# Kernel tuning notes

Measured on AMD Instinct MI355X. Metric: run time of the kernel, lower is better.

## Reference

```python
import jax, jax.numpy as jnp
import numpy as np

B, S, D = 4, 1024, 1024
H, DK, DV = 16, 64, 64


def setup_inputs() -> dict:
    key = jax.random.key(0)
    ks = jax.random.split(key, 8)
    sc = 0.02
    return {
        "queries": jax.random.normal(ks[0], (B, S, D), jnp.float32),
        "keys": jax.random.normal(ks[1], (B, S, D), jnp.float32),
        "values": jax.random.normal(ks[2], (B, S, D), jnp.float32),
        "attn_bias": jax.random.normal(ks[3], (B, 1, S, S), jnp.float32),
        "Wq": jax.random.normal(ks[4], (H * DK, D), jnp.float32) * sc,
        "Wk": jax.random.normal(ks[5], (H * DK, D), jnp.float32) * sc,
        "Wv": jax.random.normal(ks[6], (H * DV, D), jnp.float32) * sc,
        "Wp": jax.random.normal(ks[7], (D, H * DV), jnp.float32) * sc,
    }


def reference(queries, keys, values, attn_bias, Wq, Wk, Wv, Wp):
    # Linear (no bias): x @ W.T, then split heads -> [B, H, S, d]
    q = (queries @ Wq.T).reshape(B, S, H, DK).transpose(0, 2, 1, 3)
    k = (keys @ Wk.T).reshape(B, S, H, DK).transpose(0, 2, 1, 3)
    v = (values @ Wv.T).reshape(B, S, H, DV).transpose(0, 2, 1, 3)
    # NOTE: original scales by d_model**-0.5, not d_key**-0.5
    scores = jnp.einsum("bhqd,bhkd->bhqk", q, k) * (D ** -0.5)
    scores = scores + attn_bias  # bias broadcasts over heads
    weights = jax.nn.softmax(scores, axis=-1)
    out = jnp.einsum("bhqk,bhkd->bhqd", weights, v)  # [B,H,S,DV]
    out = out.transpose(0, 2, 1, 3).reshape(B, S, H * DV)
    return out @ Wp.T
```

## Files before the change

kernel.cpp:

```cpp
#include <hip/hip_runtime.h>
#include <hip/hip_bf16.h>

typedef unsigned short u16;
typedef unsigned int u32;
typedef __attribute__((ext_vector_type(8))) short bf16x8;
typedef __attribute__((ext_vector_type(8))) u16 u16x8;
typedef __attribute__((ext_vector_type(4))) u16 u16x4;
typedef __attribute__((ext_vector_type(4))) u32 u32x4;
typedef __attribute__((ext_vector_type(4))) float f32x4;
typedef __attribute__((ext_vector_type(16))) float f32x16;

typedef const __attribute__((address_space(1))) void* gas1_t;
typedef __attribute__((address_space(3))) void* las3_t;

#define MFMA16(a,b,c) __builtin_amdgcn_mfma_f32_16x16x32_bf16((a),(b),(c),0,0,0)
#define MFMA32(a,b,c) __builtin_amdgcn_mfma_f32_32x32x16_bf16((a),(b),(c),0,0,0)

static constexpr int BB = 4, SS = 1024, DD = 1024, HH = 16;

static __device__ __forceinline__ u16 f2b(float x) {
  union { __hip_bfloat16 h; u16 u; } cv;
  cv.h = __float2bfloat16(x);
  return cv.u;
}
static __device__ __forceinline__ u32 pk2(float a, float b) {
  return (u32)f2b(a) | ((u32)f2b(b) << 16);
}

__global__ __launch_bounds__(256) void cvt_all(
    const float* __restrict__ q, const float* __restrict__ k, const float* __restrict__ v,
    const float* __restrict__ wq_, const float* __restrict__ wk_, const float* __restrict__ wv_,
    const float* __restrict__ wp_,
    u16* __restrict__ qb, u16* __restrict__ kb, u16* __restrict__ vb,
    u16* __restrict__ wqb, u16* __restrict__ wkb, u16* __restrict__ wvb, u16* __restrict__ wpb) {
  int bid = blockIdx.x;
  const float* s; u16* d; int off;
  if      (bid < 4096)  { s = q;   d = qb;  off = bid; }
  else if (bid < 8192)  { s = k;   d = kb;  off = bid - 4096; }
  else if (bid < 12288) { s = v;   d = vb;  off = bid - 8192; }
  else if (bid < 13312) { s = wq_; d = wqb; off = bid - 12288; }
  else if (bid < 14336) { s = wk_; d = wkb; off = bid - 13312; }
  else if (bid < 15360) { s = wv_; d = wvb; off = bid - 14336; }
  else                  { s = wp_; d = wpb; off = bid - 15360; }
  int i = (off * 256 + threadIdx.x) * 4;
  float4 val = *(const float4*)(s + i);
  u16x4 r = { f2b(val.x), f2b(val.y), f2b(val.z), f2b(val.w) };
  *(u16x4*)(d + i) = r;
}

template<typename OT>
__global__ __launch_bounds__(256) void gemm_bt(
    const u16* __restrict__ Abase, const u16* __restrict__ Wbase, OT* __restrict__ Cbase,
    int N, int K, size_t sA, size_t sW, size_t sC) {
  const u16* A = Abase + (size_t)blockIdx.z * sA;
  const u16* W = Wbase + (size_t)blockIdx.z * sW;
  OT* C = Cbase + (size_t)blockIdx.z * sC;

  __shared__ __align__(16) u16 As[128 * 32];
  __shared__ __align__(16) u16 Bs[128 * 32];

  const int tid = threadIdx.x;
  const int lane = tid & 63;
  const int wid = tid >> 6;
  const int g = lane >> 4;
  const int li = lane & 15;
  const int brow = blockIdx.y * 128;
  const int bcol = blockIdx.x * 128;
  const int wr = (wid >> 1) * 64;
  const int wc = (wid & 1) * 64;

  const int srow = tid >> 2;
  const int scol = (tid & 3) * 8;

  f32x4 acc[4][4] = {};

  for (int k0 = 0; k0 < K; k0 += 32) {
#pragma unroll
    for (int c = 0; c < 2; ++c) {
      const u16* ga = A + (size_t)(brow + srow + c * 64) * K + k0 + scol;
      const u16* gw = W + (size_t)(bcol + srow + c * 64) * K + k0 + scol;
      __builtin_amdgcn_global_load_lds((gas1_t)(const void*)ga,
                                       (las3_t)(void*)(As + wid * 512 + c * 2048), 16, 0, 0);
      __builtin_amdgcn_global_load_lds((gas1_t)(const void*)gw,
                                       (las3_t)(void*)(Bs + wid * 512 + c * 2048), 16, 0, 0);
    }
    __syncthreads();

    bf16x8 a[4], b[4];
#pragma unroll
    for (int m = 0; m < 4; ++m)
      a[m] = *(const bf16x8*)&As[(wr + m * 16 + li) * 32 + g * 8];
#pragma unroll
    for (int n = 0; n < 4; ++n)
      b[n] = *(const bf16x8*)&Bs[(wc + n * 16 + li) * 32 + g * 8];
#pragma unroll
    for (int m = 0; m < 4; ++m)
#pragma unroll
      for (int n = 0; n < 4; ++n)
        acc[m][n] = MFMA16(a[m], b[n], acc[m][n]);
    __syncthreads();
  }

#pragma unroll
  for (int m = 0; m < 4; ++m)
#pragma unroll
    for (int n = 0; n < 4; ++n)
#pragma unroll
      for (int j = 0; j < 4; ++j) {
        int r = brow + wr + m * 16 + g * 4 + j;
        int c = bcol + wc + n * 16 + li;
        if constexpr (sizeof(OT) == 2) C[(size_t)r * N + c] = (OT)f2b(acc[m][n][j]);
        else                           C[(size_t)r * N + c] = acc[m][n][j];
      }
}

__global__ __launch_bounds__(256) void transpose_v(const u16* __restrict__ V, u16* __restrict__ Vt) {
  __shared__ __align__(16) u16 t[64][72];
  const int s0 = blockIdx.x * 64, h = blockIdx.y, b = blockIdx.z;
  const int tid = threadIdx.x;
#pragma unroll
  for (int it = 0; it < 2; ++it) {
    int slot = tid + it * 256;
    int r = slot >> 3, seg = slot & 7;
    *(u16x8*)&t[r][seg * 8] = *(const u16x8*)&V[(size_t)(b * SS + s0 + r) * DD + h * 64 + seg * 8];
  }
  __syncthreads();
#pragma unroll
  for (int it = 0; it < 2; ++it) {
    int slot = tid + it * 256;
    int dv = slot >> 3, seg = slot & 7;
    u16x8 v;
#pragma unroll
    for (int i = 0; i < 8; ++i) v[i] = t[seg * 8 + i][dv];
    *(u16x8*)&Vt[(size_t)((b * HH + h) * 64 + dv) * SS + s0 + seg * 8] = v;
  }
}

__global__ __launch_bounds__(256) void attn_kernel(
    const u16* __restrict__ Q, const u16* __restrict__ K, const u16* __restrict__ Vt,
    const float* __restrict__ bias, u16* __restrict__ O) {
  __shared__ __align__(16) u16 kbuf[2][64 * 64];
  __shared__ __align__(16) u16 vbuf[2][64 * 64];
  __shared__ float Lf[4][32];

  const int tid = threadIdx.x;
  const int lane = tid & 63;
  const int wq = tid >> 6;
  const int hi = lane >> 5;
  const int ln = lane & 31;
  const u32 swz = (u32)(ln & 7) << 4;
  const int h = blockIdx.y, b = blockIdx.z;
  const int q0 = blockIdx.x * 128;
  const int qrow = q0 + wq * 32 + ln;

  bf16x8 qf[4];
  {
    const u16* qp = Q + (size_t)(b * SS + qrow) * DD + h * 64 + hi * 8;
#pragma unroll
    for (int d = 0; d < 4; ++d) qf[d] = *(const bf16x8*)(qp + d * 16);
  }

  const int sr = tid >> 2;
  const int scb = (tid & 3) * 32;
  const u16* kg = K + (size_t)(b * SS + sr) * DD + h * 64 + scb / 2;
  const u16* vg = Vt + (size_t)((b * HH + h) * 64 + sr) * SS + scb / 2;
  const u32 wa0 = (u32)sr * 128 + (((u32)scb) ^ ((u32)(sr & 7) << 4));
  const u32 wa1 = (u32)sr * 128 + (((u32)scb + 16) ^ ((u32)(sr & 7) << 4));

  u16x8 kr0, kr1, vr0, vr1;
  kr0 = *(const u16x8*)(kg + 0);
  kr1 = *(const u16x8*)(kg + 8);
  vr0 = *(const u16x8*)(vg + 0);
  vr1 = *(const u16x8*)(vg + 8);
  *(u16x8*)((char*)kbuf[0] + wa0) = kr0;
  *(u16x8*)((char*)kbuf[0] + wa1) = kr1;
  *(u16x8*)((char*)vbuf[0] + wa0) = vr0;
  *(u16x8*)((char*)vbuf[0] + wa1) = vr1;
  __syncthreads();

  f32x16 o0 = {}, o1 = {};
  float m = -1e30f, lsum = 0.f;
  int cur = 0;

  for (int kt = 0; kt < 16; ++kt) {
    if (kt < 15) {
      const size_t k1 = (size_t)(kt + 1) * 64;
      kr0 = *(const u16x8*)(kg + k1 * DD + 0);
      kr1 = *(const u16x8*)(kg + k1 * DD + 8);
      vr0 = *(const u16x8*)(vg + k1 + 0);
      vr1 = *(const u16x8*)(vg + k1 + 8);
    }

    f32x4 bb[2][4];
    {
      const float* bp = bias + (size_t)(b * SS + qrow) * SS + kt * 64 + hi * 4;
#pragma unroll
      for (int kb = 0; kb < 2; ++kb)
#pragma unroll
        for (int rq = 0; rq < 4; ++rq)
          bb[kb][rq] = *(const f32x4*)(bp + kb * 32 + rq * 8);
    }

    const char* kb_base = (const char*)kbuf[cur];
    f32x16 s[2];
#pragma unroll
    for (int kb = 0; kb < 2; ++kb) {
      f32x16 acc = {};
#pragma unroll
      for (int d = 0; d < 4; ++d) {
        bf16x8 kf = *(const bf16x8*)(kb_base + (kb * 32 + ln) * 128 + (((u32)(d * 32 + hi * 16)) ^ swz));
        acc = MFMA32(kf, qf[d], acc);
      }
      s[kb] = acc;
    }
#pragma unroll
    for (int kb = 0; kb < 2; ++kb)
#pragma unroll
      for (int rq = 0; rq < 4; ++rq)
#pragma unroll
        for (int c = 0; c < 4; ++c)
          s[kb][rq * 4 + c] = fmaf(s[kb][rq * 4 + c], 0.03125f, bb[kb][rq][c]);

    float mt = -1e30f;
#pragma unroll
    for (int r = 0; r < 16; ++r) { mt = fmaxf(mt, s[0][r]); mt = fmaxf(mt, s[1][r]); }
    mt = fmaxf(mt, __shfl_xor(mt, 32));

    bool resc = false;
    float fsc = 1.f;
    if (kt == 0) {
      m = mt;
    } else if (__any(mt > m + 8.f)) {
      float mn = fmaxf(m, mt);
      fsc = __expf(m - mn);
      m = mn;
      resc = true;
    }

    float rs = 0.f;
    u32 w[2][8];
#pragma unroll
    for (int kb = 0; kb < 2; ++kb)
#pragma unroll
      for (int t = 0; t < 8; ++t) {
        float p0 = __expf(s[kb][2 * t] - m);
        float p1 = __expf(s[kb][2 * t + 1] - m);
        rs += p0 + p1;
        w[kb][t] = pk2(p0, p1);
      }
    rs += __shfl_xor(rs, 32);
    lsum = lsum * fsc + rs;

    if (resc) {
      if (hi == 0) Lf[wq][ln] = fsc;
#pragma unroll
      for (int rq = 0; rq < 4; ++rq) {
        f32x4 fv = *(const f32x4*)&Lf[wq][rq * 8 + hi * 4];
#pragma unroll
        for (int c = 0; c < 4; ++c) { o0[rq * 4 + c] *= fv[c]; o1[rq * 4 + c] *= fv[c]; }
      }
    }

    const char* vb_base = (const char*)vbuf[cur];
#pragma unroll
    for (int ks = 0; ks < 4; ++ks) {
      const int kb = ks >> 1, i0 = (ks & 1) * 4;
      u32 sA = hi ? w[kb][i0 + 0] : w[kb][i0 + 2];
      u32 sB = hi ? w[kb][i0 + 1] : w[kb][i0 + 3];
      u32 rA = (u32)__shfl_xor((int)sA, 32);
      u32 rB = (u32)__shfl_xor((int)sB, 32);
      u32 e0 = hi ? rA : w[kb][i0 + 0];
      u32 e1 = hi ? rB : w[kb][i0 + 1];
      u32 e2 = hi ? w[kb][i0 + 2] : rA;
      u32 e3 = hi ? w[kb][i0 + 3] : rB;
      union { u32x4 u; bf16x8 v; } pc;
      pc.u = (u32x4){e0, e1, e2, e3};
      bf16x8 pa = pc.v;
#pragma unroll
      for (int nv = 0; nv < 2; ++nv) {
        bf16x8 vf = *(const bf16x8*)(vb_base + (nv * 32 + ln) * 128 + (((u32)(ks * 32 + hi * 16)) ^ swz));
        if (nv == 0) o0 = MFMA32(pa, vf, o0);
        else         o1 = MFMA32(pa, vf, o1);
      }
    }

    if (kt < 15) {
      char* kd = (char*)kbuf[cur ^ 1];
      char* vd = (char*)vbuf[cur ^ 1];
      *(u16x8*)(kd + wa0) = kr0;
      *(u16x8*)(kd + wa1) = kr1;
      *(u16x8*)(vd + wa0) = vr0;
      *(u16x8*)(vd + wa1) = vr1;
      __syncthreads();
      cur ^= 1;
    }
  }

  float inv = 1.0f / lsum;
  if (hi == 0) Lf[wq][ln] = inv;
#pragma unroll
  for (int rq = 0; rq < 4; ++rq) {
    f32x4 iv = *(const f32x4*)&Lf[wq][rq * 8 + hi * 4];
#pragma unroll
    for (int c = 0; c < 4; ++c) {
      int q = q0 + wq * 32 + rq * 8 + hi * 4 + c;
      u16* op = O + (size_t)(b * SS + q) * DD + h * 64 + ln;
      op[0]  = f2b(o0[rq * 4 + c] * iv[c]);
      op[32] = f2b(o1[rq * 4 + c] * iv[c]);
    }
  }
}

extern "C" void kernel_launch(void* const* d_in, const int* in_sizes, int n_in,
                              void* d_out, int out_size, void* d_ws, size_t ws_size,
                              hipStream_t stream) {
  const float* queries = (const float*)d_in[0];
  const float* keys    = (const float*)d_in[1];
  const float* values  = (const float*)d_in[2];
  const float* bias    = (const float*)d_in[3];
  const float* Wq      = (const float*)d_in[4];
  const float* Wk      = (const float*)d_in[5];
  const float* Wv      = (const float*)d_in[6];
  const float* Wp      = (const float*)d_in[7];
  float* out = (float*)d_out;

  char* ws = (char*)d_ws;
  const size_t MB = 1024 * 1024;
  u16* qb  = (u16*)(ws + 0 * MB);
  u16* kb  = (u16*)(ws + 8 * MB);
  u16* vb  = (u16*)(ws + 16 * MB);
  u16* wqb = (u16*)(ws + 24 * MB);
  u16* wkb = (u16*)(ws + 26 * MB);
  u16* wvb = (u16*)(ws + 28 * MB);
  u16* wpb = (u16*)(ws + 30 * MB);
  u16* Qb  = (u16*)(ws + 32 * MB);
  u16* Kb  = (u16*)(ws + 40 * MB);
  u16* Vb  = (u16*)(ws + 48 * MB);
  u16* Vtb = (u16*)(ws + 56 * MB);
  u16* Ob  = (u16*)(ws + 0 * MB);

  const int nAct = BB * SS * DD;
  const int nW = DD * DD;

  cvt_all<<<dim3(16384), dim3(256), 0, stream>>>(
      queries, keys, values, Wq, Wk, Wv, Wp,
      qb, kb, vb, wqb, wkb, wvb, wpb);

  gemm_bt<u16><<<dim3(8, 32, 3), dim3(256), 0, stream>>>(
      qb, wqb, Qb, DD, DD, (size_t)nAct, (size_t)nW, (size_t)nAct);

  transpose_v<<<dim3(16, 16, 4), dim3(256), 0, stream>>>(Vb, Vtb);

  attn_kernel<<<dim3(8, 16, 4), dim3(256), 0, stream>>>(Qb, Kb, Vtb, bias, Ob);

  gemm_bt<float><<<dim3(8, 32, 1), dim3(256), 0, stream>>>(
      Ob, wpb, out, DD, DD, 0, 0, 0);
}
```

Measured before the change: 139.8 us.

## Prefetch attention bias one tile ahead and streamline softmax arithmetic

The attention bias tile for the next key block is now loaded into registers one iteration early, alongside the K/V prefetch, instead of right before use, so its global-memory latency is hidden. The softmax now uses exp2 with a folded log2e multiply-add, tree reductions for the row max and row sum, and a packed bf16 convert instruction in place of two scalar conversions. MFMA sections are wrapped in s_setprio raises to favour matrix issue across waves. The cost is an extra 32 live VGPRs for the prefetched bias, which may lower occupancy.

```diff
diff --git a/kernel.cpp b/kernel.cpp
--- a/kernel.cpp
+++ b/kernel.cpp
@@ -1,5 +1,6 @@
 #include <hip/hip_runtime.h>
 #include <hip/hip_bf16.h>
+#include <cmath>
 
 typedef unsigned short u16;
 typedef unsigned int u32;
@@ -23,8 +24,13 @@
   cv.h = __float2bfloat16(x);
   return cv.u;
 }
-static __device__ __forceinline__ u32 pk2(float a, float b) {
-  return (u32)f2b(a) | ((u32)f2b(b) << 16);
+static __device__ __forceinline__ u32 cvtpk(float lo, float hi) {
+  u32 r;
+  asm("v_cvt_pk_bf16_f32 %0, %1, %2" : "=v"(r) : "v"(lo), "v"(hi));
+  return r;
+}
+static __device__ __forceinline__ float fmax3(float a, float b, float c) {
+  return fmaxf(fmaxf(a, b), c);
 }
 
 __global__ __launch_bounds__(256) void cvt_all(
@@ -176,11 +182,21 @@
   *(u16x8*)((char*)kbuf[0] + wa1) = kr1;
   *(u16x8*)((char*)vbuf[0] + wa0) = vr0;
   *(u16x8*)((char*)vbuf[0] + wa1) = vr1;
+
+  const float* bp = bias + (size_t)(b * SS + qrow) * SS + hi * 4;
+  f32x4 bb[2][4], bbn[2][4];
+#pragma unroll
+  for (int kb = 0; kb < 2; ++kb)
+#pragma unroll
+    for (int rq = 0; rq < 4; ++rq)
+      bb[kb][rq] = *(const f32x4*)(bp + kb * 32 + rq * 8);
+
   __syncthreads();
 
   f32x16 o0 = {}, o1 = {};
   float m = -1e30f, lsum = 0.f;
   int cur = 0;
+  const float L2E = 1.4426950408889634f;
 
   for (int kt = 0; kt < 16; ++kt) {
     if (kt < 15) {
@@ -189,20 +205,17 @@
       kr1 = *(const u16x8*)(kg + k1 * DD + 8);
       vr0 = *(const u16x8*)(vg + k1 + 0);
       vr1 = *(const u16x8*)(vg + k1 + 8);
-    }
-
-    f32x4 bb[2][4];
-    {
-      const float* bp = bias + (size_t)(b * SS + qrow) * SS + kt * 64 + hi * 4;
+      const float* bp1 = bp + (kt + 1) * 64;
 #pragma unroll
       for (int kb = 0; kb < 2; ++kb)
 #pragma unroll
         for (int rq = 0; rq < 4; ++rq)
-          bb[kb][rq] = *(const f32x4*)(bp + kb * 32 + rq * 8);
+          bbn[kb][rq] = *(const f32x4*)(bp1 + kb * 32 + rq * 8);
     }
 
     const char* kb_base = (const char*)kbuf[cur];
     f32x16 s[2];
+    __builtin_amdgcn_s_setprio(1);
 #pragma unroll
     for (int kb = 0; kb < 2; ++kb) {
       f32x16 acc = {};
@@ -213,6 +226,8 @@
       }
       s[kb] = acc;
     }
+    __builtin_amdgcn_s_setprio(0);
+
 #pragma unroll
     for (int kb = 0; kb < 2; ++kb)
 #pragma unroll
@@ -221,9 +236,12 @@
         for (int c = 0; c < 4; ++c)
           s[kb][rq * 4 + c] = fmaf(s[kb][rq * 4 + c], 0.03125f, bb[kb][rq][c]);
 
-    float mt = -1e30f;
-#pragma unroll
-    for (int r = 0; r < 16; ++r) { mt = fmaxf(mt, s[0][r]); mt = fmaxf(mt, s[1][r]); }
+    float r8[8];
+#pragma unroll
+    for (int i = 0; i < 8; ++i)
+      r8[i] = fmaxf(fmaxf(s[0][i], s[0][i + 8]), fmaxf(s[1][i], s[1][i + 8]));
+    float mt = fmaxf(fmax3(r8[0], r8[1], r8[2]),
+                     fmax3(fmax3(r8[3], r8[4], r8[5]), r8[6], r8[7]));
     mt = fmaxf(mt, __shfl_xor(mt, 32));
 
     bool resc = false;
@@ -237,19 +255,28 @@
       resc = true;
     }
 
-    float rs = 0.f;
-    u32 w[2][8];
+    const float mneg = -m * L2E;
+    float p[2][16];
 #pragma unroll
     for (int kb = 0; kb < 2; ++kb)
 #pragma unroll
-      for (int t = 0; t < 8; ++t) {
-        float p0 = __expf(s[kb][2 * t] - m);
-        float p1 = __expf(s[kb][2 * t + 1] - m);
-        rs += p0 + p1;
-        w[kb][t] = pk2(p0, p1);
-      }
+      for (int i = 0; i < 16; ++i)
+        p[kb][i] = exp2f(fmaf(s[kb][i], L2E, mneg));
+
+    float t8[8];
+#pragma unroll
+    for (int i = 0; i < 8; ++i)
+      t8[i] = (p[0][i] + p[0][i + 8]) + (p[1][i] + p[1][i + 8]);
+    float rs = ((t8[0] + t8[1]) + (t8[2] + t8[3])) + ((t8[4] + t8[5]) + (t8[6] + t8[7]));
     rs += __shfl_xor(rs, 32);
     lsum = lsum * fsc + rs;
+
+    u32 w[2][8];
+#pragma unroll
+    for (int kb = 0; kb < 2; ++kb)
+#pragma unroll
+      for (int t = 0; t < 8; ++t)
+        w[kb][t] = cvtpk(p[kb][2 * t], p[kb][2 * t + 1]);
 
     if (resc) {
       if (hi == 0) Lf[wq][ln] = fsc;
@@ -276,12 +303,14 @@
       union { u32x4 u; bf16x8 v; } pc;
       pc.u = (u32x4){e0, e1, e2, e3};
       bf16x8 pa = pc.v;
+      __builtin_amdgcn_s_setprio(1);
 #pragma unroll
       for (int nv = 0; nv < 2; ++nv) {
         bf16x8 vf = *(const bf16x8*)(vb_base + (nv * 32 + ln) * 128 + (((u32)(ks * 32 + hi * 16)) ^ swz));
         if (nv == 0) o0 = MFMA32(pa, vf, o0);
         else         o1 = MFMA32(pa, vf, o1);
       }
+      __builtin_amdgcn_s_setprio(0);
     }
 
     if (kt < 15) {
@@ -293,6 +322,11 @@
       *(u16x8*)(vd + wa1) = vr1;
       __syncthreads();
       cur ^= 1;
+#pragma unroll
+      for (int kb = 0; kb < 2; ++kb)
+#pragma unroll
+        for (int rq = 0; rq < 4; ++rq)
+          bb[kb][rq] = bbn[kb][rq];
     }
   }
 
```

Result: slower. 142.9 us (+2.3%).

## Split attention KV range across two wave groups with LDS merge and block remap

Applied to the files above, without the earlier changes.

The attention kernel now runs 512 threads per block: two groups of four waves each process half of the key sequence (512 keys each) for the same 128 query rows. The two partial softmax states are merged through shared memory at the end. The block index is also remapped so that neighbouring blocks handle different batch/head/tile combinations, and s_setprio is raised around the MFMA sections. This doubles the waves per block and halves the serial loop length, to hide latency and improve occupancy, at the cost of more LDS, an extra merge step with barriers, and half the waves idling during the epilogue.

```diff
diff --git a/kernel.cpp b/kernel.cpp
--- a/kernel.cpp
+++ b/kernel.cpp
@@ -136,22 +136,26 @@
   }
 }
 
-__global__ __launch_bounds__(256) void attn_kernel(
+__global__ __launch_bounds__(512) void attn_kernel(
     const u16* __restrict__ Q, const u16* __restrict__ K, const u16* __restrict__ Vt,
     const float* __restrict__ bias, u16* __restrict__ O) {
-  __shared__ __align__(16) u16 kbuf[2][64 * 64];
-  __shared__ __align__(16) u16 vbuf[2][64 * 64];
-  __shared__ float Lf[4][32];
+  __shared__ __align__(16) u16 smem[8 * 4096];
+  __shared__ float Lf[8][32];
 
   const int tid = threadIdx.x;
   const int lane = tid & 63;
-  const int wq = tid >> 6;
+  const int wid = tid >> 6;
+  const int g2 = tid >> 8;
+  const int wqq = wid & 3;
   const int hi = lane >> 5;
   const int ln = lane & 31;
   const u32 swz = (u32)(ln & 7) << 4;
-  const int h = blockIdx.y, b = blockIdx.z;
-  const int q0 = blockIdx.x * 128;
-  const int qrow = q0 + wq * 32 + ln;
+
+  const int flat = blockIdx.x + (blockIdx.y << 3) + (blockIdx.z << 7);
+  const int w = ((flat & 7) << 6) | (flat >> 3);
+  const int qt = w & 7, h = (w >> 3) & 15, b = w >> 7;
+  const int q0 = qt * 128;
+  const int qrow = q0 + wqq * 32 + ln;
 
   bf16x8 qf[4];
   {
@@ -160,10 +164,11 @@
     for (int d = 0; d < 4; ++d) qf[d] = *(const bf16x8*)(qp + d * 16);
   }
 
-  const int sr = tid >> 2;
-  const int scb = (tid & 3) * 32;
-  const u16* kg = K + (size_t)(b * SS + sr) * DD + h * 64 + scb / 2;
-  const u16* vg = Vt + (size_t)((b * HH + h) * 64 + sr) * SS + scb / 2;
+  const int t8 = tid & 255;
+  const int sr = t8 >> 2;
+  const int scb = (t8 & 3) * 32;
+  const u16* kg = K + (size_t)(b * SS + g2 * 512 + sr) * DD + h * 64 + scb / 2;
+  const u16* vg = Vt + (size_t)((b * HH + h) * 64 + sr) * SS + g2 * 512 + scb / 2;
   const u32 wa0 = (u32)sr * 128 + (((u32)scb) ^ ((u32)(sr & 7) << 4));
   const u32 wa1 = (u32)sr * 128 + (((u32)scb + 16) ^ ((u32)(sr & 7) << 4));
 
@@ -172,18 +177,24 @@
   kr1 = *(const u16x8*)(kg + 8);
   vr0 = *(const u16x8*)(vg + 0);
   vr1 = *(const u16x8*)(vg + 8);
-  *(u16x8*)((char*)kbuf[0] + wa0) = kr0;
-  *(u16x8*)((char*)kbuf[0] + wa1) = kr1;
-  *(u16x8*)((char*)vbuf[0] + wa0) = vr0;
-  *(u16x8*)((char*)vbuf[0] + wa1) = vr1;
+  {
+    char* kd = (char*)(smem + (g2 * 4 + 0) * 4096);
+    char* vd = (char*)(smem + (g2 * 4 + 2) * 4096);
+    *(u16x8*)(kd + wa0) = kr0;
+    *(u16x8*)(kd + wa1) = kr1;
+    *(u16x8*)(vd + wa0) = vr0;
+    *(u16x8*)(vd + wa1) = vr1;
+  }
   __syncthreads();
+
+  const float* bp = bias + (size_t)(b * SS + qrow) * SS + g2 * 512 + hi * 4;
 
   f32x16 o0 = {}, o1 = {};
   float m = -1e30f, lsum = 0.f;
   int cur = 0;
 
-  for (int kt = 0; kt < 16; ++kt) {
-    if (kt < 15) {
+  for (int kt = 0; kt < 8; ++kt) {
+    if (kt < 7) {
       const size_t k1 = (size_t)(kt + 1) * 64;
       kr0 = *(const u16x8*)(kg + k1 * DD + 0);
       kr1 = *(const u16x8*)(kg + k1 * DD + 8);
@@ -193,16 +204,17 @@
 
     f32x4 bb[2][4];
     {
-      const float* bp = bias + (size_t)(b * SS + qrow) * SS + kt * 64 + hi * 4;
+      const float* bpt = bp + kt * 64;
 #pragma unroll
       for (int kb = 0; kb < 2; ++kb)
 #pragma unroll
         for (int rq = 0; rq < 4; ++rq)
-          bb[kb][rq] = *(const f32x4*)(bp + kb * 32 + rq * 8);
-    }
-
-    const char* kb_base = (const char*)kbuf[cur];
+          bb[kb][rq] = *(const f32x4*)(bpt + kb * 32 + rq * 8);
+    }
+
+    const char* kb_base = (const char*)(smem + (g2 * 4 + 0 + cur) * 4096);
     f32x16 s[2];
+    __builtin_amdgcn_s_setprio(1);
 #pragma unroll
     for (int kb = 0; kb < 2; ++kb) {
       f32x16 acc = {};
@@ -213,6 +225,8 @@
       }
       s[kb] = acc;
     }
+    __builtin_amdgcn_s_setprio(0);
+
 #pragma unroll
     for (int kb = 0; kb < 2; ++kb)
 #pragma unroll
@@ -238,7 +252,7 @@
     }
 
     float rs = 0.f;
-    u32 w[2][8];
+    u32 wv[2][8];
 #pragma unroll
     for (int kb = 0; kb < 2; ++kb)
 #pragma unroll
@@ -246,47 +260,49 @@
         float p0 = __expf(s[kb][2 * t] - m);
         float p1 = __expf(s[kb][2 * t + 1] - m);
         rs += p0 + p1;
-        w[kb][t] = pk2(p0, p1);
+        wv[kb][t] = pk2(p0, p1);
       }
     rs += __shfl_xor(rs, 32);
     lsum = lsum * fsc + rs;
 
     if (resc) {
-      if (hi == 0) Lf[wq][ln] = fsc;
+      if (hi == 0) Lf[wid][ln] = fsc;
 #pragma unroll
       for (int rq = 0; rq < 4; ++rq) {
-        f32x4 fv = *(const f32x4*)&Lf[wq][rq * 8 + hi * 4];
+        f32x4 fv = *(const f32x4*)&Lf[wid][rq * 8 + hi * 4];
 #pragma unroll
         for (int c = 0; c < 4; ++c) { o0[rq * 4 + c] *= fv[c]; o1[rq * 4 + c] *= fv[c]; }
       }
     }
 
-    const char* vb_base = (const char*)vbuf[cur];
+    const char* vb_base = (const char*)(smem + (g2 * 4 + 2 + cur) * 4096);
 #pragma unroll
     for (int ks = 0; ks < 4; ++ks) {
       const int kb = ks >> 1, i0 = (ks & 1) * 4;
-      u32 sA = hi ? w[kb][i0 + 0] : w[kb][i0 + 2];
-      u32 sB = hi ? w[kb][i0 + 1] : w[kb][i0 + 3];
+      u32 sA = hi ? wv[kb][i0 + 0] : wv[kb][i0 + 2];
+      u32 sB = hi ? wv[kb][i0 + 1] : wv[kb][i0 + 3];
       u32 rA = (u32)__shfl_xor((int)sA, 32);
       u32 rB = (u32)__shfl_xor((int)sB, 32);
-      u32 e0 = hi ? rA : w[kb][i0 + 0];
-      u32 e1 = hi ? rB : w[kb][i0 + 1];
-      u32 e2 = hi ? w[kb][i0 + 2] : rA;
-      u32 e3 = hi ? w[kb][i0 + 3] : rB;
+      u32 e0 = hi ? rA : wv[kb][i0 + 0];
+      u32 e1 = hi ? rB : wv[kb][i0 + 1];
+      u32 e2 = hi ? wv[kb][i0 + 2] : rA;
+      u32 e3 = hi ? wv[kb][i0 + 3] : rB;
       union { u32x4 u; bf16x8 v; } pc;
       pc.u = (u32x4){e0, e1, e2, e3};
       bf16x8 pa = pc.v;
+      __builtin_amdgcn_s_setprio(1);
 #pragma unroll
       for (int nv = 0; nv < 2; ++nv) {
         bf16x8 vf = *(const bf16x8*)(vb_base + (nv * 32 + ln) * 128 + (((u32)(ks * 32 + hi * 16)) ^ swz));
         if (nv == 0) o0 = MFMA32(pa, vf, o0);
         else         o1 = MFMA32(pa, vf, o1);
       }
-    }
-
-    if (kt < 15) {
-      char* kd = (char*)kbuf[cur ^ 1];
-      char* vd = (char*)vbuf[cur ^ 1];
+      __builtin_amdgcn_s_setprio(0);
+    }
+
+    if (kt < 7) {
+      char* kd = (char*)(smem + (g2 * 4 + 0 + (cur ^ 1)) * 4096);
+      char* vd = (char*)(smem + (g2 * 4 + 2 + (cur ^ 1)) * 4096);
       *(u16x8*)(kd + wa0) = kr0;
       *(u16x8*)(kd + wa1) = kr1;
       *(u16x8*)(vd + wa0) = vr0;
@@ -296,17 +312,50 @@
     }
   }
 
-  float inv = 1.0f / lsum;
-  if (hi == 0) Lf[wq][ln] = inv;
-#pragma unroll
-  for (int rq = 0; rq < 4; ++rq) {
-    f32x4 iv = *(const f32x4*)&Lf[wq][rq * 8 + hi * 4];
-#pragma unroll
-    for (int c = 0; c < 4; ++c) {
-      int q = q0 + wq * 32 + rq * 8 + hi * 4 + c;
-      u16* op = O + (size_t)(b * SS + q) * DD + h * 64 + ln;
-      op[0]  = f2b(o0[rq * 4 + c] * iv[c]);
-      op[32] = f2b(o1[rq * 4 + c] * iv[c]);
+  float* scr = (float*)smem;
+  __syncthreads();
+  if (wid >= 4) {
+    float* sc = scr + ((wid - 4) * 36) * 64 + lane;
+#pragma unroll
+    for (int j = 0; j < 16; ++j) sc[j * 64] = o0[j];
+#pragma unroll
+    for (int j = 0; j < 16; ++j) sc[(16 + j) * 64] = o1[j];
+    sc[32 * 64] = m;
+    sc[33 * 64] = lsum;
+  }
+  __syncthreads();
+  if (wid < 4) {
+    float* sc = scr + (wid * 36) * 64 + lane;
+    float m_b = sc[32 * 64];
+    float l_b = sc[33 * 64];
+    float mn = fmaxf(m, m_b);
+    float al = __expf(m - mn);
+    float be = __expf(m_b - mn);
+    lsum = lsum * al + l_b * be;
+    if (hi == 0) { Lf[wid][ln] = al; Lf[wid + 4][ln] = be; }
+#pragma unroll
+    for (int rq = 0; rq < 4; ++rq) {
+      f32x4 av = *(const f32x4*)&Lf[wid][rq * 8 + hi * 4];
+      f32x4 bv = *(const f32x4*)&Lf[wid + 4][rq * 8 + hi * 4];
+#pragma unroll
+      for (int c = 0; c < 4; ++c) {
+        o0[rq * 4 + c] = o0[rq * 4 + c] * av[c] + sc[(rq * 4 + c) * 64] * bv[c];
+        o1[rq * 4 + c] = o1[rq * 4 + c] * av[c] + sc[(16 + rq * 4 + c) * 64] * bv[c];
+      }
+    }
+
+    float inv = 1.0f / lsum;
+    if (hi == 0) Lf[wid][ln] = inv;
+#pragma unroll
+    for (int rq = 0; rq < 4; ++rq) {
+      f32x4 iv = *(const f32x4*)&Lf[wid][rq * 8 + hi * 4];
+#pragma unroll
+      for (int c = 0; c < 4; ++c) {
+        int q = q0 + wid * 32 + rq * 8 + hi * 4 + c;
+        u16* op = O + (size_t)(b * SS + q) * DD + h * 64 + ln;
+        op[0]  = f2b(o0[rq * 4 + c] * iv[c]);
+        op[32] = f2b(o1[rq * 4 + c] * iv[c]);
+      }
     }
   }
 }
@@ -351,7 +400,7 @@
 
   transpose_v<<<dim3(16, 16, 4), dim3(256), 0, stream>>>(Vb, Vtb);
 
-  attn_kernel<<<dim3(8, 16, 4), dim3(256), 0, stream>>>(Qb, Kb, Vtb, bias, Ob);
+  attn_kernel<<<dim3(8, 16, 4), dim3(512), 0, stream>>>(Qb, Kb, Vtb, bias, Ob);
 
   gemm_bt<float><<<dim3(8, 32, 1), dim3(256), 0, stream>>>(
       Ob, wpb, out, DD, DD, 0, 0, 0);
```

Measured after the change: 149.9 us. 1.07x slower.

## Split attention KV range in two with partial outputs and a merge kernel

Applied to the files above, without the earlier changes.

Each attention block now handles half of the key sequence, doubling the grid from 512 to 1024 blocks. Each half writes unnormalised fp16 partial outputs plus its row max and sum, and a new merge kernel combines the two halves into the bf16 output. The block index is also remapped so neighbouring blocks work on different query tiles and heads. The aim is better occupancy across the GPU's compute units, at the cost of an extra kernel launch, extra memory traffic for the partials, and fp16 range risk on the unnormalised accumulators.

```diff
diff --git a/kernel.cpp b/kernel.cpp
--- a/kernel.cpp
+++ b/kernel.cpp
@@ -5,6 +5,7 @@
 typedef unsigned int u32;
 typedef __attribute__((ext_vector_type(8))) short bf16x8;
 typedef __attribute__((ext_vector_type(8))) u16 u16x8;
+typedef __attribute__((ext_vector_type(8))) _Float16 f16x8;
 typedef __attribute__((ext_vector_type(4))) u16 u16x4;
 typedef __attribute__((ext_vector_type(4))) u32 u32x4;
 typedef __attribute__((ext_vector_type(4))) float f32x4;
@@ -138,7 +139,10 @@
 
 __global__ __launch_bounds__(256) void attn_kernel(
     const u16* __restrict__ Q, const u16* __restrict__ K, const u16* __restrict__ Vt,
-    const float* __restrict__ bias, u16* __restrict__ O) {
+    const float* __restrict__ bias,
+    _Float16* __restrict__ Op0, _Float16* __restrict__ Op1,
+    float* __restrict__ mp0, float* __restrict__ lp0,
+    float* __restrict__ mp1, float* __restrict__ lp1) {
   __shared__ __align__(16) u16 kbuf[2][64 * 64];
   __shared__ __align__(16) u16 vbuf[2][64 * 64];
   __shared__ float Lf[4][32];
@@ -149,9 +153,17 @@
   const int hi = lane >> 5;
   const int ln = lane & 31;
   const u32 swz = (u32)(ln & 7) << 4;
-  const int h = blockIdx.y, b = blockIdx.z;
-  const int q0 = blockIdx.x * 128;
+
+  const int flat = blockIdx.x + (blockIdx.y << 3) + (blockIdx.z << 7);
+  const int L = ((flat & 7) << 7) | (flat >> 3);
+  const int qt = L & 7, h = (L >> 3) & 15, bz = L >> 7;
+  const int b = bz >> 1, g2 = bz & 1;
+  const int q0 = qt * 128;
   const int qrow = q0 + wq * 32 + ln;
+
+  _Float16* Op = g2 ? Op1 : Op0;
+  float* mp = g2 ? mp1 : mp0;
+  float* lp = g2 ? lp1 : lp0;
 
   bf16x8 qf[4];
   {
@@ -162,8 +174,8 @@
 
   const int sr = tid >> 2;
   const int scb = (tid & 3) * 32;
-  const u16* kg = K + (size_t)(b * SS + sr) * DD + h * 64 + scb / 2;
-  const u16* vg = Vt + (size_t)((b * HH + h) * 64 + sr) * SS + scb / 2;
+  const u16* kg = K + (size_t)(b * SS + g2 * 512 + sr) * DD + h * 64 + scb / 2;
+  const u16* vg = Vt + (size_t)((b * HH + h) * 64 + sr) * SS + g2 * 512 + scb / 2;
   const u32 wa0 = (u32)sr * 128 + (((u32)scb) ^ ((u32)(sr & 7) << 4));
   const u32 wa1 = (u32)sr * 128 + (((u32)scb + 16) ^ ((u32)(sr & 7) << 4));
 
@@ -178,12 +190,14 @@
   *(u16x8*)((char*)vbuf[0] + wa1) = vr1;
   __syncthreads();
 
+  const float* bp = bias + (size_t)(b * SS + qrow) * SS + g2 * 512 + hi * 4;
+
   f32x16 o0 = {}, o1 = {};
   float m = -1e30f, lsum = 0.f;
   int cur = 0;
 
-  for (int kt = 0; kt < 16; ++kt) {
-    if (kt < 15) {
+  for (int kt = 0; kt < 8; ++kt) {
+    if (kt < 7) {
       const size_t k1 = (size_t)(kt + 1) * 64;
       kr0 = *(const u16x8*)(kg + k1 * DD + 0);
       kr1 = *(const u16x8*)(kg + k1 * DD + 8);
@@ -193,12 +207,12 @@
 
     f32x4 bb[2][4];
     {
-      const float* bp = bias + (size_t)(b * SS + qrow) * SS + kt * 64 + hi * 4;
+      const float* bpt = bp + kt * 64;
 #pragma unroll
       for (int kb = 0; kb < 2; ++kb)
 #pragma unroll
         for (int rq = 0; rq < 4; ++rq)
-          bb[kb][rq] = *(const f32x4*)(bp + kb * 32 + rq * 8);
+          bb[kb][rq] = *(const f32x4*)(bpt + kb * 32 + rq * 8);
     }
 
     const char* kb_base = (const char*)kbuf[cur];
@@ -238,7 +252,7 @@
     }
 
     float rs = 0.f;
-    u32 w[2][8];
+    u32 wv[2][8];
 #pragma unroll
     for (int kb = 0; kb < 2; ++kb)
 #pragma unroll
@@ -246,7 +260,7 @@
         float p0 = __expf(s[kb][2 * t] - m);
         float p1 = __expf(s[kb][2 * t + 1] - m);
         rs += p0 + p1;
-        w[kb][t] = pk2(p0, p1);
+        wv[kb][t] = pk2(p0, p1);
       }
     rs += __shfl_xor(rs, 32);
     lsum = lsum * fsc + rs;
@@ -265,14 +279,14 @@
 #pragma unroll
     for (int ks = 0; ks < 4; ++ks) {
       const int kb = ks >> 1, i0 = (ks & 1) * 4;
-      u32 sA = hi ? w[kb][i0 + 0] : w[kb][i0 + 2];
-      u32 sB = hi ? w[kb][i0 + 1] : w[kb][i0 + 3];
+      u32 sA = hi ? wv[kb][i0 + 0] : wv[kb][i0 + 2];
+      u32 sB = hi ? wv[kb][i0 + 1] : wv[kb][i0 + 3];
       u32 rA = (u32)__shfl_xor((int)sA, 32);
       u32 rB = (u32)__shfl_xor((int)sB, 32);
-      u32 e0 = hi ? rA : w[kb][i0 + 0];
-      u32 e1 = hi ? rB : w[kb][i0 + 1];
-      u32 e2 = hi ? w[kb][i0 + 2] : rA;
-      u32 e3 = hi ? w[kb][i0 + 3] : rB;
+      u32 e0 = hi ? rA : wv[kb][i0 + 0];
+      u32 e1 = hi ? rB : wv[kb][i0 + 1];
+      u32 e2 = hi ? wv[kb][i0 + 2] : rA;
+      u32 e3 = hi ? wv[kb][i0 + 3] : rB;
       union { u32x4 u; bf16x8 v; } pc;
       pc.u = (u32x4){e0, e1, e2, e3};
       bf16x8 pa = pc.v;
@@ -284,7 +298,7 @@
       }
     }
 
-    if (kt < 15) {
+    if (kt < 7) {
       char* kd = (char*)kbuf[cur ^ 1];
       char* vd = (char*)vbuf[cur ^ 1];
       *(u16x8*)(kd + wa0) = kr0;
@@ -296,19 +310,46 @@
     }
   }
 
-  float inv = 1.0f / lsum;
-  if (hi == 0) Lf[wq][ln] = inv;
+  const size_t rbase = (size_t)(b * HH + h) * SS;
+  if (hi == 0) {
+    mp[rbase + qrow] = m;
+    lp[rbase + qrow] = lsum;
+  }
 #pragma unroll
   for (int rq = 0; rq < 4; ++rq) {
-    f32x4 iv = *(const f32x4*)&Lf[wq][rq * 8 + hi * 4];
 #pragma unroll
     for (int c = 0; c < 4; ++c) {
       int q = q0 + wq * 32 + rq * 8 + hi * 4 + c;
-      u16* op = O + (size_t)(b * SS + q) * DD + h * 64 + ln;
-      op[0]  = f2b(o0[rq * 4 + c] * iv[c]);
-      op[32] = f2b(o1[rq * 4 + c] * iv[c]);
-    }
-  }
+      _Float16* op = Op + (rbase + q) * 64 + ln;
+      op[0]  = (_Float16)o0[rq * 4 + c];
+      op[32] = (_Float16)o1[rq * 4 + c];
+    }
+  }
+}
+
+__global__ __launch_bounds__(256) void merge_kernel(
+    const _Float16* __restrict__ Op0, const _Float16* __restrict__ Op1,
+    const float* __restrict__ mp0, const float* __restrict__ lp0,
+    const float* __restrict__ mp1, const float* __restrict__ lp1,
+    u16* __restrict__ Ob) {
+  const int tid = threadIdx.x;
+  const int row = blockIdx.x * 32 + (tid >> 3);
+  const int dvg = (tid & 7) * 8;
+  float m0 = mp0[row], m1 = mp1[row];
+  float l0 = lp0[row], l1 = lp1[row];
+  float mn = fmaxf(m0, m1);
+  float e0 = __expf(m0 - mn), e1 = __expf(m1 - mn);
+  float inv = 1.0f / (l0 * e0 + l1 * e1);
+  float f0 = e0 * inv, f1 = e1 * inv;
+  f16x8 p0 = *(const f16x8*)(Op0 + (size_t)row * 64 + dvg);
+  f16x8 p1 = *(const f16x8*)(Op1 + (size_t)row * 64 + dvg);
+  const int b = row >> 14, h = (row >> 10) & 15, q = row & 1023;
+  u16* dst = Ob + (size_t)(b * SS + q) * DD + h * 64 + dvg;
+  u16x8 r;
+#pragma unroll
+  for (int j = 0; j < 8; ++j)
+    r[j] = f2b((float)p0[j] * f0 + (float)p1[j] * f1);
+  *(u16x8*)dst = r;
 }
 
 extern "C" void kernel_launch(void* const* d_in, const int* in_sizes, int n_in,
@@ -337,6 +378,12 @@
   u16* Kb  = (u16*)(ws + 40 * MB);
   u16* Vb  = (u16*)(ws + 48 * MB);
   u16* Vtb = (u16*)(ws + 56 * MB);
+  _Float16* Op0 = (_Float16*)(ws + 8 * MB);
+  _Float16* Op1 = (_Float16*)(ws + 17 * MB);
+  float* mp0 = (float*)(ws + 26 * MB);
+  float* lp0 = (float*)(ws + 26 * MB + 256 * 1024);
+  float* mp1 = (float*)(ws + 26 * MB + 512 * 1024);
+  float* lp1 = (float*)(ws + 26 * MB + 768 * 1024);
   u16* Ob  = (u16*)(ws + 0 * MB);
 
   const int nAct = BB * SS * DD;
@@ -351,7 +398,11 @@
 
   transpose_v<<<dim3(16, 16, 4), dim3(256), 0, stream>>>(Vb, Vtb);
 
-  attn_kernel<<<dim3(8, 16, 4), dim3(256), 0, stream>>>(Qb, Kb, Vtb, bias, Ob);
+  attn_kernel<<<dim3(8, 16, 8), dim3(256), 0, stream>>>(
+      Qb, Kb, Vtb, bias, Op0, Op1, mp0, lp0, mp1, lp1);
+
+  merge_kernel<<<dim3(2048), dim3(256), 0, stream>>>(
+      Op0, Op1, mp0, lp0, mp1, lp1, Ob);
 
   gemm_bt<float><<<dim3(8, 32, 1), dim3(256), 0, stream>>>(
       Ob, wpb, out, DD, DD, 0, 0, 0);
```

Result: slower. 146.4 us (+4.7%).
